# Kernel optimization log

Hardware: AMD Instinct MI355X
Metric: run time of the kernel (lower is better)

## Reference

```python
import jax, jax.numpy as jnp
import numpy as np

B, LATENT = 8192, 1024
NR, NC = 12, 12                      # nb_rows, nb_cols
H0, W0 = NR + 2, NC + 2              # 14x14 after reshape
EPS = 1e-5
SLOPE = 0.01                         # LeakyReLU default


def setup_inputs() -> dict:
    key = jax.random.key(0)
    ks = jax.random.split(key, 9)
    s = 0.05
    return {
        "x": jax.random.normal(ks[0], (B, LATENT), jnp.float32),
        "fc_w": jax.random.normal(ks[1], (H0 * W0 * 36, LATENT), jnp.float32) * s,
        "fc_b": jax.random.normal(ks[2], (H0 * W0 * 36,), jnp.float32) * s,
        "conv_w": jax.random.normal(ks[3], (16, 36, 2, 2), jnp.float32) * s,
        "conv_b": jax.random.normal(ks[4], (16,), jnp.float32) * s,
        "gamma": jnp.ones((16,), jnp.float32),
        "beta": jnp.zeros((16,), jnp.float32),
        # locally-connected weights: (out_ch, in_ch, Hout, Wout, k*k)
        "lw1": jax.random.normal(ks[5], (6, 16, H0 - 1, W0 - 1, 4), jnp.float32) * s,
        "lw2": jax.random.normal(ks[6], (1, 6, H0 - 2, W0 - 2, 4), jnp.float32) * s,
    }


def _leaky(x):
    return jnp.where(x >= 0, x, SLOPE * x)


def _local_conv2(x, w):
    # x: (B,C,H,W); w: (O,C,Ho,Wo,4) with k=2, stride 1, no padding
    Ho, Wo = w.shape[2], w.shape[3]
    patches = jnp.stack(
        [x[:, :, dy:dy + Ho, dx:dx + Wo] for dy in (0, 1) for dx in (0, 1)],
        axis=-1)  # (B,C,Ho,Wo,4)
    return jnp.einsum('bchwk,ochwk->bohw', patches, w)


def reference(x, fc_w, fc_b, conv_w, conv_b, gamma, beta, lw1, lw2):
    # fc -> view(B, H0, W0, 36) -> permute to NCHW
    h = x @ fc_w.T + fc_b
    h = h.reshape(B, H0, W0, 36).transpose(0, 3, 1, 2)  # (B,36,14,14)
    # Conv2d k=2 padding='same' (torch pads bottom/right for even kernels)
    h = jax.lax.conv_general_dilated(
        h, conv_w, window_strides=(1, 1), padding=((0, 1), (0, 1)),
        dimension_numbers=('NCHW', 'OIHW', 'NCHW')) + conv_b[None, :, None, None]
    h = _leaky(h)
    # BatchNorm2d (training mode: batch stats, biased var)
    mu = h.mean(axis=(0, 2, 3), keepdims=True)
    var = h.var(axis=(0, 2, 3), keepdims=True)
    h = (h - mu) * jax.lax.rsqrt(var + EPS)
    h = h * gamma[None, :, None, None] + beta[None, :, None, None]
    # locally-connected stack: 14x14 -> 13x13 -> 12x12
    h = _leaky(_local_conv2(h, lw1))
    return _local_conv2(h, lw2)  # (B,1,12,12)
```

## Files before the change

### kernel.cpp

```cpp
#include <hip/hip_runtime.h>


#define SLOPE 0.01f

typedef __bf16 bf16x8 __attribute__((ext_vector_type(8)));
typedef float f32x4 __attribute__((ext_vector_type(4)));

typedef const __attribute__((address_space(1))) void* gas_ptr;
typedef __attribute__((address_space(3))) void* las_ptr;

__device__ __forceinline__ void load16_to_lds(const void* g, void* l) {
  __builtin_amdgcn_global_load_lds((gas_ptr)g, (las_ptr)l, 16, 0, 0);
}

__device__ __forceinline__ unsigned short f2bf(float f) {
  union { float f; unsigned int u; } v; v.f = f;
  unsigned int r = v.u + 0x7FFFu + ((v.u >> 16) & 1u);
  return (unsigned short)(r >> 16);
}
__device__ __forceinline__ float bfbits2f(unsigned int bits16) {
  union { unsigned int u; float f; } v; v.u = bits16 << 16;
  return v.f;
}
__device__ __forceinline__ float leaky(float v) { return v >= 0.f ? v : SLOPE * v; }

__global__ void k_cast_x(const float* __restrict__ x, unsigned short* __restrict__ xb,
                         float* __restrict__ stats) {
  if (blockIdx.x == 0 && threadIdx.x < 32) stats[threadIdx.x] = 0.f;
  int gid = blockIdx.x * 256 + threadIdx.x;
  const float4* x4 = (const float4*)x;
  float4 a = x4[gid * 2], b = x4[gid * 2 + 1];
  union { unsigned short s[8]; uint4 v; } o;
  o.s[0] = f2bf(a.x); o.s[1] = f2bf(a.y); o.s[2] = f2bf(a.z); o.s[3] = f2bf(a.w);
  o.s[4] = f2bf(b.x); o.s[5] = f2bf(b.y); o.s[6] = f2bf(b.z); o.s[7] = f2bf(b.w);
  ((uint4*)xb)[gid] = o.v;
}

__global__ void k_fold(const float* __restrict__ fc_w, const float* __restrict__ fc_b,
                       const float* __restrict__ conv_w, const float* __restrict__ conv_b,
                       unsigned short* __restrict__ Wc, float* __restrict__ bc) {
  __shared__ float cw[2304];
  int blk = blockIdx.x, kg = blockIdx.y, t = threadIdx.x;
  if (blk == 196) {
    if (kg != 0) return;
    uint4 z = make_uint4(0, 0, 0, 0);
    uint4* dst = (uint4*)(Wc + 3136 * 1024);
    for (int i = t; i < 8192; i += 256) dst[i] = z;
    for (int i = 3136 + t; i < 3200; i += 256) bc[i] = 0.f;
    return;
  }
  for (int i = t; i < 2304; i += 256) cw[i] = conv_w[i];
  __syncthreads();
  int i0 = blk / 14, j0 = blk - (blk / 14) * 14;
  int kcol = kg * 256 + t;
  float acc[16];
#pragma unroll
  for (int o = 0; o < 16; o++) acc[o] = 0.f;
  for (int c = 0; c < 36; c++) {
#pragma unroll
    for (int dy = 0; dy < 2; dy++) {
      int ii = i0 + dy; if (ii > 13) continue;
#pragma unroll
      for (int dx = 0; dx < 2; dx++) {
        int jj = j0 + dx; if (jj > 13) continue;
        int row = (ii * 14 + jj) * 36 + c;
        float f = fc_w[row * 1024 + kcol];
        int kk = dy * 2 + dx;
#pragma unroll
        for (int o = 0; o < 16; o++)
          acc[o] += cw[(o * 36 + c) * 4 + kk] * f;
      }
    }
  }
#pragma unroll
  for (int o = 0; o < 16; o++) {
    int n = o * 196 + i0 * 14 + j0;
    Wc[n * 1024 + kcol] = f2bf(acc[o]);
  }
  if (kg == 0 && t < 16) {
    int o = t;
    float b = conv_b[o];
    for (int c = 0; c < 36; c++)
      for (int dy = 0; dy < 2; dy++) {
        int ii = i0 + dy; if (ii > 13) continue;
        for (int dx = 0; dx < 2; dx++) {
          int jj = j0 + dx; if (jj > 13) continue;
          b += cw[(o * 36 + c) * 4 + dy * 2 + dx] * fc_b[(ii * 14 + jj) * 36 + c];
        }
      }
    bc[o * 196 + i0 * 14 + j0] = b;
  }
}

__global__ __launch_bounds__(256, 4) void k_gemm(const unsigned short* __restrict__ Xb,
                                                 const unsigned short* __restrict__ Wcb,
                                                 const float* __restrict__ bc,
                                                 unsigned short* __restrict__ h2,
                                                 float* __restrict__ stats) {
  __shared__ __align__(16) char lds[16384];
  __shared__ float red[4][4];
  const int t = threadIdx.x;
  const int w = t >> 6, lane = t & 63;
  const int quad = lane >> 4, l15 = lane & 15;
  const int bid = blockIdx.x;
  const int xcd = bid & 7, j = bid >> 3;
  const int mblk = xcd * 8 + (j & 7);
  const int nblk = j >> 3;
  const int m0 = mblk * 128, n0 = nblk * 128;
  const int mrow = t & 127, tko = t >> 7;
  const unsigned short* ga = Xb + (m0 + mrow) * 1024 + tko * 8;
  const unsigned short* gb = Wcb + (n0 + mrow) * 1024 + tko * 8;
  char* lA = lds;
  char* lB = lds + 8192;
  const int wbase = w * 1024;
  const int wm0 = (w >> 1) * 64, wn0 = (w & 1) * 64;

  f32x4 acc[4][4];
#pragma unroll
  for (int a = 0; a < 4; a++)
#pragma unroll
    for (int b = 0; b < 4; b++) acc[a][b] = (f32x4){0.f, 0.f, 0.f, 0.f};

  for (int kb = 0; kb < 1024; kb += 32) {
    __syncthreads();
    load16_to_lds(ga + kb,      lA + wbase);
    load16_to_lds(ga + kb + 16, lA + 4096 + wbase);
    load16_to_lds(gb + kb,      lB + wbase);
    load16_to_lds(gb + kb + 16, lB + 4096 + wbase);
    __syncthreads();

    bf16x8 af[4], bfr[4];
#pragma unroll
    for (int mb = 0; mb < 4; mb++)
      af[mb] = *(const bf16x8*)(lA + quad * 2048 + (wm0 + mb * 16 + l15) * 16);
#pragma unroll
    for (int nb = 0; nb < 4; nb++)
      bfr[nb] = *(const bf16x8*)(lB + quad * 2048 + (wn0 + nb * 16 + l15) * 16);
#pragma unroll
    for (int mb = 0; mb < 4; mb++)
#pragma unroll
      for (int nb = 0; nb < 4; nb++)
        acc[mb][nb] = __builtin_amdgcn_mfma_f32_16x16x32_bf16(af[mb], bfr[nb], acc[mb][nb], 0, 0, 0);
  }

  const int cLo = n0 / 196;
  const int cHi = (n0 + 127) / 196;
  float ss0 = 0.f, ss1 = 0.f, sq0 = 0.f, sq1 = 0.f;
#pragma unroll
  for (int nb = 0; nb < 4; nb++) {
    int col = n0 + wn0 + nb * 16 + l15;
    float bias = bc[col];
    int ch = col / 196;
    bool hi = (ch != cLo);
    bool valid = col < 3136;
    float cs = 0.f, cq = 0.f;
#pragma unroll
    for (int mb = 0; mb < 4; mb++) {
#pragma unroll
      for (int r = 0; r < 4; r++) {
        int row = m0 + wm0 + mb * 16 + quad * 4 + r;
        float v = leaky(acc[mb][nb][r] + bias);
        h2[row * 3200 + col] = f2bf(v);
        cs += v; cq += v * v;
      }
    }
    if (valid) {
      if (hi) { ss1 += cs; sq1 += cq; } else { ss0 += cs; sq0 += cq; }
    }
  }
#pragma unroll
  for (int off = 1; off < 64; off <<= 1) {
    ss0 += __shfl_xor(ss0, off, 64);
    ss1 += __shfl_xor(ss1, off, 64);
    sq0 += __shfl_xor(sq0, off, 64);
    sq1 += __shfl_xor(sq1, off, 64);
  }
  if (lane == 0) { red[w][0] = ss0; red[w][1] = ss1; red[w][2] = sq0; red[w][3] = sq1; }
  __syncthreads();
  if (t == 0) {
    float a0 = red[0][0] + red[1][0] + red[2][0] + red[3][0];
    float a1 = red[0][1] + red[1][1] + red[2][1] + red[3][1];
    float b0 = red[0][2] + red[1][2] + red[2][2] + red[3][2];
    float b1 = red[0][3] + red[1][3] + red[2][3] + red[3][3];
    atomicAdd(&stats[cLo], a0);
    atomicAdd(&stats[16 + cLo], b0);
    if (cHi != cLo && cHi < 16) {
      atomicAdd(&stats[cHi], a1);
      atomicAdd(&stats[16 + cHi], b1);
    }
  }
}

__global__ __launch_bounds__(256) void k_tail(const unsigned short* __restrict__ h2,
                                              const float* __restrict__ stats,
                                              const float* __restrict__ gamma,
                                              const float* __restrict__ beta,
                                              const float* __restrict__ lw1,
                                              const float* __restrict__ lw2,
                                              float* __restrict__ out) {
  __shared__ unsigned short h3[4 * 3138];
  __shared__ float h4[4 * 1015];
  __shared__ float sc[16], sh[16];
  int b0 = blockIdx.x * 4, t = threadIdx.x;
  if (t < 16) {
    const float inv = 1.f / 1605632.f;
    float mean = stats[t] * inv;
    float var = stats[16 + t] * inv - mean * mean;
    float rstd = rsqrtf(var + 1e-5f);
    float s = gamma[t] * rstd;
    sc[t] = s; sh[t] = beta[t] - mean * s;
  }
  __syncthreads();
  for (int i = t; i < 6272; i += 256) {
    int bb = i / 1568, q = i - bb * 1568;
    int n = q * 2, o = n / 196;
    unsigned int u = *(const unsigned int*)(h2 + (b0 + bb) * 3200 + n);
    float v0 = bfbits2f(u & 0xffffu) * sc[o] + sh[o];
    float v1 = bfbits2f(u >> 16) * sc[o] + sh[o];
    unsigned int pk = (unsigned int)f2bf(v0) | ((unsigned int)f2bf(v1) << 16);
    *(unsigned int*)(h3 + bb * 3138 + n) = pk;
  }
  __syncthreads();
  for (int u = t; u < 156; u += 256) {
    int rp = u & 1, rest = u >> 1;
    int o = rest / 13, y = rest - o * 13;
    int rA = 2 * rp, rB = 2 * rp + 1;
    float acc0[13], acc1[13];
#pragma unroll
    for (int x = 0; x < 13; x++) { acc0[x] = 0.f; acc1[x] = 0.f; }
    const unsigned short* hA = h3 + rA * 3138;
    const unsigned short* hB = h3 + rB * 3138;
    for (int c = 0; c < 16; c++) {
      float a0[14], a1[14], e0[14], e1[14];
      const unsigned int* pA0 = (const unsigned int*)(hA + c * 196 + y * 14);
      const unsigned int* pA1 = (const unsigned int*)(hA + c * 196 + (y + 1) * 14);
      const unsigned int* pB0 = (const unsigned int*)(hB + c * 196 + y * 14);
      const unsigned int* pB1 = (const unsigned int*)(hB + c * 196 + (y + 1) * 14);
#pragma unroll
      for (int q = 0; q < 7; q++) {
        unsigned int vA0 = pA0[q], vA1 = pA1[q], vB0 = pB0[q], vB1 = pB1[q];
        a0[2 * q] = bfbits2f(vA0 & 0xffffu); a0[2 * q + 1] = bfbits2f(vA0 >> 16);
        a1[2 * q] = bfbits2f(vA1 & 0xffffu); a1[2 * q + 1] = bfbits2f(vA1 >> 16);
        e0[2 * q] = bfbits2f(vB0 & 0xffffu); e0[2 * q + 1] = bfbits2f(vB0 >> 16);
        e1[2 * q] = bfbits2f(vB1 & 0xffffu); e1[2 * q + 1] = bfbits2f(vB1 >> 16);
      }
      const float4* wp4 = (const float4*)(lw1 + (((o * 16 + c) * 13 + y) * 13) * 4);
#pragma unroll
      for (int x = 0; x < 13; x++) {
        float4 wv = wp4[x];
        acc0[x] += a0[x] * wv.x + a0[x + 1] * wv.y + a1[x] * wv.z + a1[x + 1] * wv.w;
        acc1[x] += e0[x] * wv.x + e0[x + 1] * wv.y + e1[x] * wv.z + e1[x + 1] * wv.w;
      }
    }
#pragma unroll
    for (int x = 0; x < 13; x++) {
      h4[rA * 1015 + (o * 13 + y) * 13 + x] = leaky(acc0[x]);
      h4[rB * 1015 + (o * 13 + y) * 13 + x] = leaky(acc1[x]);
    }
  }
  __syncthreads();
  for (int oi = t; oi < 576; oi += 256) {
    int pos = oi >> 2, bb = oi & 3;
    int y = pos / 12, x = pos - y * 12;
    float a = 0.f;
    const float* hp = h4 + bb * 1015;
    const float4* w4 = (const float4*)lw2;
#pragma unroll
    for (int c = 0; c < 6; c++) {
      float4 wv = w4[(c * 12 + y) * 12 + x];
      int hb = c * 169 + y * 13 + x;
      a += hp[hb] * wv.x + hp[hb + 1] * wv.y +
           hp[hb + 13] * wv.z + hp[hb + 14] * wv.w;
    }
    out[(b0 + bb) * 144 + pos] = a;
  }
}

extern "C" void kernel_launch(void* const* d_in, const int* in_sizes, int n_in,
                              void* d_out, int out_size, void* d_ws, size_t ws_size,
                              hipStream_t stream) {
  const float* x      = (const float*)d_in[0];
  const float* fc_w   = (const float*)d_in[1];
  const float* fc_b   = (const float*)d_in[2];
  const float* conv_w = (const float*)d_in[3];
  const float* conv_b = (const float*)d_in[4];
  const float* gamma  = (const float*)d_in[5];
  const float* beta   = (const float*)d_in[6];
  const float* lw1    = (const float*)d_in[7];
  const float* lw2    = (const float*)d_in[8];

  char* ws = (char*)d_ws;
  unsigned short* Xb    = (unsigned short*)(ws);
  unsigned short* Wc    = (unsigned short*)(ws + 16777216);
  float*          bc    = (float*)(ws + 23330816);
  float*          stats = (float*)(ws + 23343616);
  unsigned short* h2    = (unsigned short*)(ws + 23343744);

  k_cast_x<<<4096, 256, 0, stream>>>(x, Xb, stats);
  k_fold<<<dim3(197, 4), 256, 0, stream>>>(fc_w, fc_b, conv_w, conv_b, Wc, bc);
  k_gemm<<<1600, 256, 0, stream>>>(Xb, Wc, bc, h2, stats);
  k_tail<<<2048, 256, 0, stream>>>(h2, stats, gamma, beta, lw1, lw2, (float*)d_out);
}
```

Baseline: 371.0 us.

## Double-buffer GEMM LDS loads and merge cast and fold kernels

The GEMM main loop now uses two LDS buffers. The next K-slice is issued with global_load_lds while the current one is computed, and the code waits with vmcnt(4) instead of a full sync before each step. Separately, the x-cast and weight-fold kernels are merged into one launch to save a kernel launch and let the two overlap. Doubling LDS to 32KB per block may lower occupancy under launch_bounds(256,4). Correctness depends on the vmcnt count matching the outstanding loads.

```diff
diff --git a/kernel.cpp b/kernel.cpp
--- a/kernel.cpp
+++ b/kernel.cpp
@@ -24,23 +24,26 @@
 }
 __device__ __forceinline__ float leaky(float v) { return v >= 0.f ? v : SLOPE * v; }
 
-__global__ void k_cast_x(const float* __restrict__ x, unsigned short* __restrict__ xb,
-                         float* __restrict__ stats) {
-  if (blockIdx.x == 0 && threadIdx.x < 32) stats[threadIdx.x] = 0.f;
-  int gid = blockIdx.x * 256 + threadIdx.x;
-  const float4* x4 = (const float4*)x;
-  float4 a = x4[gid * 2], b = x4[gid * 2 + 1];
-  union { unsigned short s[8]; uint4 v; } o;
-  o.s[0] = f2bf(a.x); o.s[1] = f2bf(a.y); o.s[2] = f2bf(a.z); o.s[3] = f2bf(a.w);
-  o.s[4] = f2bf(b.x); o.s[5] = f2bf(b.y); o.s[6] = f2bf(b.z); o.s[7] = f2bf(b.w);
-  ((uint4*)xb)[gid] = o.v;
-}
-
-__global__ void k_fold(const float* __restrict__ fc_w, const float* __restrict__ fc_b,
+__global__ void k_prep(const float* __restrict__ x, unsigned short* __restrict__ xb,
+                       const float* __restrict__ fc_w, const float* __restrict__ fc_b,
                        const float* __restrict__ conv_w, const float* __restrict__ conv_b,
-                       unsigned short* __restrict__ Wc, float* __restrict__ bc) {
+                       unsigned short* __restrict__ Wc, float* __restrict__ bc,
+                       float* __restrict__ stats) {
   __shared__ float cw[2304];
-  int blk = blockIdx.x, kg = blockIdx.y, t = threadIdx.x;
+  const int bid = blockIdx.x, t = threadIdx.x;
+  if (bid < 4096) {
+    if (bid == 0 && t < 32) stats[t] = 0.f;
+    int gid = bid * 256 + t;
+    const float4* x4 = (const float4*)x;
+    float4 a = x4[gid * 2], b = x4[gid * 2 + 1];
+    union { unsigned short s[8]; uint4 v; } o;
+    o.s[0] = f2bf(a.x); o.s[1] = f2bf(a.y); o.s[2] = f2bf(a.z); o.s[3] = f2bf(a.w);
+    o.s[4] = f2bf(b.x); o.s[5] = f2bf(b.y); o.s[6] = f2bf(b.z); o.s[7] = f2bf(b.w);
+    ((uint4*)xb)[gid] = o.v;
+    return;
+  }
+  const int r = bid - 4096;
+  const int blk = r % 197, kg = r / 197;
   if (blk == 196) {
     if (kg != 0) return;
     uint4 z = make_uint4(0, 0, 0, 0);
@@ -97,7 +100,7 @@
                                                  const float* __restrict__ bc,
                                                  unsigned short* __restrict__ h2,
                                                  float* __restrict__ stats) {
-  __shared__ __align__(16) char lds[16384];
+  __shared__ __align__(16) char lds[32768];
   __shared__ float red[4][4];
   const int t = threadIdx.x;
   const int w = t >> 6, lane = t & 63;
@@ -110,8 +113,6 @@
   const int mrow = t & 127, tko = t >> 7;
   const unsigned short* ga = Xb + (m0 + mrow) * 1024 + tko * 8;
   const unsigned short* gb = Wcb + (n0 + mrow) * 1024 + tko * 8;
-  char* lA = lds;
-  char* lB = lds + 8192;
   const int wbase = w * 1024;
   const int wm0 = (w >> 1) * 64, wn0 = (w & 1) * 64;
 
@@ -121,14 +122,17 @@
 #pragma unroll
     for (int b = 0; b < 4; b++) acc[a][b] = (f32x4){0.f, 0.f, 0.f, 0.f};
 
-  for (int kb = 0; kb < 1024; kb += 32) {
-    __syncthreads();
-    load16_to_lds(ga + kb,      lA + wbase);
-    load16_to_lds(ga + kb + 16, lA + 4096 + wbase);
-    load16_to_lds(gb + kb,      lB + wbase);
-    load16_to_lds(gb + kb + 16, lB + 4096 + wbase);
-    __syncthreads();
-
+  auto stage = [&](int buf, int kb) {
+    char* sA = lds + buf * 16384;
+    char* sB = sA + 8192;
+    load16_to_lds(ga + kb,      sA + wbase);
+    load16_to_lds(ga + kb + 16, sA + 4096 + wbase);
+    load16_to_lds(gb + kb,      sB + wbase);
+    load16_to_lds(gb + kb + 16, sB + 4096 + wbase);
+  };
+  auto compute = [&](int buf) {
+    const char* lA = lds + buf * 16384;
+    const char* lB = lA + 8192;
     bf16x8 af[4], bfr[4];
 #pragma unroll
     for (int mb = 0; mb < 4; mb++)
@@ -141,7 +145,21 @@
 #pragma unroll
       for (int nb = 0; nb < 4; nb++)
         acc[mb][nb] = __builtin_amdgcn_mfma_f32_16x16x32_bf16(af[mb], bfr[nb], acc[mb][nb], 0, 0, 0);
-  }
+  };
+
+  stage(0, 0);
+  int cur = 0;
+  for (int kb = 0; kb < 992; kb += 32) {
+    stage(cur ^ 1, kb + 32);
+    asm volatile("s_waitcnt vmcnt(4)" ::: "memory");
+    __builtin_amdgcn_s_barrier();
+    compute(cur);
+    __builtin_amdgcn_s_barrier();
+    cur ^= 1;
+  }
+  asm volatile("s_waitcnt vmcnt(0)" ::: "memory");
+  __builtin_amdgcn_s_barrier();
+  compute(cur);
 
   const int cLo = n0 / 196;
   const int cHi = (n0 + 127) / 196;
@@ -296,8 +314,7 @@
   float*          stats = (float*)(ws + 23343616);
   unsigned short* h2    = (unsigned short*)(ws + 23343744);
 
-  k_cast_x<<<4096, 256, 0, stream>>>(x, Xb, stats);
-  k_fold<<<dim3(197, 4), 256, 0, stream>>>(fc_w, fc_b, conv_w, conv_b, Wc, bc);
+  k_prep<<<4884, 256, 0, stream>>>(x, Xb, fc_w, fc_b, conv_w, conv_b, Wc, bc, stats);
   k_gemm<<<1600, 256, 0, stream>>>(Xb, Wc, bc, h2, stats);
   k_tail<<<2048, 256, 0, stream>>>(h2, stats, gamma, beta, lw1, lw2, (float*)d_out);
 }
```

Result: slower. 394.5 us (+6.3%).
